# Optimization experiments

Hardware: AMD Instinct MI355X
Metric: run time of the kernel (lower is better)

The kernel has to match this reference:

```python
import jax, jax.numpy as jnp
import numpy as np

B, T, D, S = 64, 577, 768, 577  # batch, seq, hidden, v-out (=seq of e)


def setup_inputs() -> dict:
    key = jax.random.key(0)
    ks = jax.random.split(key, 8)
    sc = 1.0 / np.sqrt(D)
    return {
        "b": jax.random.normal(ks[0], (B, T, D), jnp.float32),
        "e": jax.random.normal(ks[1], (B, T, D), jnp.float32),
        "Wq": jax.random.normal(ks[2], (D, D), jnp.float32) * sc,
        "bq": jnp.zeros((D,), jnp.float32),
        "Wk": jax.random.normal(ks[3], (D, D), jnp.float32) * sc,
        "bk": jnp.zeros((D,), jnp.float32),
        "Wv": jax.random.normal(ks[4], (S, D), jnp.float32) * sc,
        "bv": jnp.zeros((S,), jnp.float32),
    }


def reference(b, e, Wq, bq, Wk, bk, Wv, bv):
    # Dropout layers are identity in eval mode.
    q = b @ Wq.T + bq                      # [B,T,D]
    k = e @ Wk.T + bk                      # [B,S,D]
    v = b @ Wv.T + bv                      # [B,T,S]
    # tanh(Q K^T) @ V^T : [B,T,S] @ [B,S,T] -> [B,T,T]
    attn = jnp.tanh(jnp.einsum("btd,bsd->bts", q, k))
    out = jnp.einsum("bts,bus->btu", attn, v)
    return out  # squeeze is a no-op for B>1
```

## Files before the change

### kernel.cpp

```cpp
#include <hip/hip_runtime.h>
#include <hip/hip_fp16.h>


typedef _Float16 f16x8 __attribute__((ext_vector_type(8)));
typedef _Float16 f16x4 __attribute__((ext_vector_type(4)));
typedef float f32x4 __attribute__((ext_vector_type(4)));

__global__ void cvt8_kernel(const float* __restrict__ src, _Float16* __restrict__ dst,
                            long long n8) {
    long long i = blockIdx.x * (long long)blockDim.x + threadIdx.x;
    const long long stride = gridDim.x * (long long)blockDim.x;
    for (; i < n8; i += stride) {
        const float4 f0 = ((const float4*)src)[2 * i];
        const float4 f1 = ((const float4*)src)[2 * i + 1];
        f16x8 h;
        h[0] = (_Float16)f0.x; h[1] = (_Float16)f0.y; h[2] = (_Float16)f0.z; h[3] = (_Float16)f0.w;
        h[4] = (_Float16)f1.x; h[5] = (_Float16)f1.y; h[6] = (_Float16)f1.z; h[7] = (_Float16)f1.w;
        ((f16x8*)dst)[i] = h;
    }
}

__global__ void cvtT2_kernel(const float* __restrict__ s0, _Float16* __restrict__ d0,
                             const float* __restrict__ s1, _Float16* __restrict__ d1) {
    __shared__ float t[32][33];
    const float* src = blockIdx.z ? s1 : s0;
    _Float16* dst = blockIdx.z ? d1 : d0;
    const int bx = blockIdx.x, by = blockIdx.y;
    const int tx = threadIdx.x & 31, ty = threadIdx.x >> 5;
#pragma unroll
    for (int k = 0; k < 4; ++k) {
        const int r = ty + 8 * k;
        t[r][tx] = src[(size_t)(by * 32 + r) * 768 + bx * 32 + tx];
    }
    __syncthreads();
#pragma unroll
    for (int k = 0; k < 4; ++k) {
        const int r = ty + 8 * k;
        dst[(size_t)(bx * 32 + r) * 768 + by * 32 + tx] = (_Float16)t[tx][r];
    }
}

__global__ void prep_kernel(const _Float16* __restrict__ WqT, const _Float16* __restrict__ WkT,
                            const float* __restrict__ bq, const float* __restrict__ bk,
                            const float* __restrict__ bv,
                            float* __restrict__ w2f, _Float16* __restrict__ Mt_aug,
                            float* __restrict__ bias_mg) {
    const int wid = blockIdx.x * 4 + (threadIdx.x >> 6);
    const int lane = threadIdx.x & 63;
    if (wid < 768) {
        float s = 0.f;
        for (int k = 0; k < 12; ++k) s += (float)WqT[(size_t)wid * 768 + lane + 64 * k] * bk[lane + 64 * k];
        for (int o = 32; o; o >>= 1) s += __shfl_xor(s, o);
        if (lane == 0) Mt_aug[(size_t)768 * 768 + wid] = (_Float16)s;
    } else if (wid < 1536) {
        const int n = wid - 768;
        float s = 0.f;
        for (int k = 0; k < 12; ++k) s += (float)WkT[(size_t)n * 768 + lane + 64 * k] * bq[lane + 64 * k];
        for (int o = 32; o; o >>= 1) s += __shfl_xor(s, o);
        if (lane == 0) w2f[n] = s;
    } else if (wid == 1536) {
        float s = 0.f;
        for (int k = 0; k < 12; ++k) s += bq[lane + 64 * k] * bk[lane + 64 * k];
        for (int o = 32; o; o >>= 1) s += __shfl_xor(s, o);
        if (lane < 32) {
            float v = 0.f;
            if (lane == 0) v = s;
            if (lane == 1) v = 1.f;
            bias_mg[768 + lane] = v;
        }
    } else if (wid < 1560) {
        const int i = (wid - 1537) * 64 + lane;
        if (i < 768) bias_mg[i] = 0.f;
        else {
            const int j = i + 32;
            if (j < 1408) bias_mg[j] = (j < 1377) ? bv[j - 800] : 0.f;
        }
    } else if (wid < 1591) {
        const int r = 769 + (wid - 1560);
        for (int k = 0; k < 12; ++k) Mt_aug[(size_t)r * 768 + lane + 64 * k] = (_Float16)0.f;
    }
}

__global__ void cvt_e_aug_kernel(const float* __restrict__ e, const float* __restrict__ w2f,
                                 _Float16* __restrict__ dst, int rows) {
    const int wpb = blockDim.x >> 6;
    int wid = blockIdx.x * wpb + (threadIdx.x >> 6);
    const int nw = gridDim.x * wpb;
    const int lane = threadIdx.x & 63;
    for (int s = wid; s < rows; s += nw) {
        const float4* er = (const float4*)(e + (size_t)s * 768);
        _Float16* dr = dst + (size_t)s * 800;
        float dot = 0.f;
#pragma unroll
        for (int k = 0; k < 3; ++k) {
            const int idx = lane + 64 * k;
            const float4 v = er[idx];
            const float4 w = ((const float4*)w2f)[idx];
            dot += v.x * w.x + v.y * w.y + v.z * w.z + v.w * w.w;
            f16x4 h;
            h[0] = (_Float16)v.x; h[1] = (_Float16)v.y;
            h[2] = (_Float16)v.z; h[3] = (_Float16)v.w;
            *(f16x4*)(dr + 4 * idx) = h;
        }
        for (int o = 32; o; o >>= 1) dot += __shfl_xor(dot, o);
        if (lane < 32) {
            _Float16 v = (_Float16)0.f;
            if (lane == 0) v = (_Float16)1.f;
            if (lane == 1) v = (_Float16)dot;
            dr[768 + lane] = v;
        }
    }
}

__device__ __forceinline__ void gload16(const _Float16* g, _Float16* l) {
    __builtin_amdgcn_global_load_lds(
        (const __attribute__((address_space(1))) unsigned int*)(g),
        (__attribute__((address_space(3))) unsigned int*)(l),
        16, 0, 0);
}

__device__ __forceinline__ float fast_tanh(float x) {
    const float t = __builtin_amdgcn_exp2f(2.885390081777927f * x);
    return 1.f - 2.f * __builtin_amdgcn_rcpf(t + 1.f);
}

template<bool TANH, bool OUT_F16, bool BIAS, int MODE>
__global__ __launch_bounds__(256)
void gemm_nt_f16(const _Float16* __restrict__ A, const _Float16* __restrict__ Bt,
                 const float* __restrict__ bias, void* __restrict__ Cp,
                 int M, int Nreal, int Nstore, int K,
                 int lda, int ldb, int ldc, int nTileN, int nTiles,
                 long long sA, long long sB, long long sC)
{
    __shared__ __align__(16) _Float16 lds[3 * 8192];

    int bid = blockIdx.x;
    int z, tm, tn;
    if (MODE == 0) {
        const int nwg = gridDim.x;
        const int q8 = nwg >> 3, r8 = nwg & 7;
        const int xcd = bid & 7, loc = bid >> 3;
        bid = (xcd < r8 ? xcd * (q8 + 1) : r8 * (q8 + 1) + (xcd - r8) * q8) + loc;
        z = 0;
        tm = bid / nTileN; tn = bid - tm * nTileN;
    } else {
        const int xcd = bid & 7, idx = bid >> 3;
        const int g = idx / nTiles, tile = idx - g * nTiles;
        z = g * 8 + xcd;
        tm = tile / nTileN; tn = tile - tm * nTileN;
    }
    const int m0 = tm << 7, n0 = tn << 7;

    const _Float16* Az = A + (size_t)z * sA;
    const _Float16* Bz = Bt + (size_t)z * sB;

    const int tid = threadIdx.x;
    const int lane = tid & 63;
    const int wid = tid >> 6;
    const int wm = wid >> 1, wn = wid & 1;

    const int r0 = tid >> 2;
    const int c0 = (((tid & 3) ^ ((tid >> 3) & 3)) << 3);
    const int rA0 = (m0 + r0      < M ? m0 + r0      : M - 1);
    const int rA1 = (m0 + r0 + 64 < M ? m0 + r0 + 64 : M - 1);
    const int rB0 = (n0 + r0      < Nreal ? n0 + r0      : Nreal - 1);
    const int rB1 = (n0 + r0 + 64 < Nreal ? n0 + r0 + 64 : Nreal - 1);
    const _Float16* pA0 = Az + (size_t)rA0 * lda + c0;
    const _Float16* pA1 = Az + (size_t)rA1 * lda + c0;
    const _Float16* pB0 = Bz + (size_t)rB0 * ldb + c0;
    const _Float16* pB1 = Bz + (size_t)rB1 * ldb + c0;

    const int o0 = tid * 8, o1 = (tid + 256) * 8;

    const int rr = lane & 15;
    const int hh = lane >> 4;
    const int sw = (rr >> 1) & 3;
    const int fAo = ((wm * 64 + rr) * 4 + (hh ^ sw)) * 8;
    const int fBo = ((wn * 64 + rr) * 4 + (hh ^ sw)) * 8;

    const f32x4 z4 = {0.f, 0.f, 0.f, 0.f};
    f32x4 acc[4][4];
#pragma unroll
    for (int i = 0; i < 4; ++i)
#pragma unroll
        for (int j = 0; j < 4; ++j) acc[i][j] = z4;

    const int nt = K >> 5;

#define STAGE(si, kt)                                              \
    do {                                                           \
        _Float16* base_ = lds + (si) * 8192;                       \
        const int ko_ = (kt) << 5;                                 \
        gload16(pA0 + ko_, base_ + o0);                            \
        gload16(pA1 + ko_, base_ + o1);                            \
        gload16(pB0 + ko_, base_ + 4096 + o0);                     \
        gload16(pB1 + ko_, base_ + 4096 + o1);                     \
    } while (0)

#define COMPUTE(si)                                                            \
    do {                                                                       \
        const _Float16* cA_ = lds + (si) * 8192;                               \
        const _Float16* cB_ = cA_ + 4096;                                      \
        f16x8 a_[4], b_[4];                                                    \
        _Pragma("unroll")                                                      \
        for (int mi = 0; mi < 4; ++mi) a_[mi] = *(const f16x8*)(cA_ + fAo + mi * 512); \
        _Pragma("unroll")                                                      \
        for (int ni = 0; ni < 4; ++ni) b_[ni] = *(const f16x8*)(cB_ + fBo + ni * 512); \
        _Pragma("unroll")                                                      \
        for (int mi = 0; mi < 4; ++mi)                                         \
            _Pragma("unroll")                                                  \
            for (int ni = 0; ni < 4; ++ni)                                     \
                acc[mi][ni] = __builtin_amdgcn_mfma_f32_16x16x32_f16(          \
                    a_[mi], b_[ni], acc[mi][ni], 0, 0, 0);                     \
    } while (0)

    STAGE(0, 0);
    STAGE(1, 1);

    for (int j = 0; j < nt - 1; ++j) {
        asm volatile("s_waitcnt vmcnt(4)" ::: "memory");
        __builtin_amdgcn_s_barrier();
        __builtin_amdgcn_sched_barrier(0);
        if (j + 2 < nt) STAGE((j + 2) % 3, j + 2);
        COMPUTE(j % 3);
    }
    asm volatile("s_waitcnt vmcnt(0)" ::: "memory");
    __builtin_amdgcn_s_barrier();
    __builtin_amdgcn_sched_barrier(0);
    COMPUTE((nt - 1) % 3);

#undef STAGE
#undef COMPUTE

    const int cr0 = (lane >> 4) << 2;
    const int cc = lane & 15;
    float*    Cf = (float*)Cp    + (size_t)z * sC;
    _Float16* Ch = (_Float16*)Cp + (size_t)z * sC;
#pragma unroll
    for (int mi = 0; mi < 4; ++mi) {
#pragma unroll
        for (int ni = 0; ni < 4; ++ni) {
            const int gc = n0 + wn * 64 + ni * 16 + cc;
            if (gc >= Nstore) continue;
            const bool real = gc < Nreal;
            float bb = 0.f;
            if (BIAS) bb = real ? bias[gc] : 0.f;
#pragma unroll
            for (int r = 0; r < 4; ++r) {
                const int gr = m0 + wm * 64 + mi * 16 + cr0 + r;
                if (gr >= M) continue;
                float x = real ? (acc[mi][ni][r] + bb) : 0.f;
                if (TANH) x = fast_tanh(x);
                if (OUT_F16) Ch[(size_t)gr * ldc + gc] = (_Float16)x;
                else         Cf[(size_t)gr * ldc + gc] = x;
            }
        }
    }
}

extern "C" void kernel_launch(void* const* d_in, const int* in_sizes, int n_in,
                              void* d_out, int out_size, void* d_ws, size_t ws_size,
                              hipStream_t stream)
{
    const float* b  = (const float*)d_in[0];
    const float* e  = (const float*)d_in[1];
    const float* Wq = (const float*)d_in[2];
    const float* bq = (const float*)d_in[3];
    const float* Wk = (const float*)d_in[4];
    const float* bk = (const float*)d_in[5];
    const float* Wv = (const float*)d_in[6];
    const float* bv = (const float*)d_in[7];
    float* out = (float*)d_out;

    const int BT = 36928, T = 577, S = 577, Sp = 608, Kb = 800;
    const int Nmg = 1408;

    _Float16* WqT_h  = (_Float16*)d_ws;
    _Float16* WkT_h  = WqT_h + 589824;
    _Float16* Mt_aug = WkT_h + 589824;
    _Float16* Wv_h   = Mt_aug + 614400;
    float*    bias_mg = (float*)(Wv_h + 443136);
    float*    w2f     = (float*)((_Float16*)bias_mg + 2816);
    _Float16* S1    = (_Float16*)w2f + 1536;
    _Float16* S_big = S1 + (size_t)BT * Kb;
    _Float16* S4    = S_big + (size_t)BT * Nmg;

    cvtT2_kernel<<<dim3(24, 24, 2), 256, 0, stream>>>(Wq, WqT_h, Wk, WkT_h);
    cvt8_kernel<<<217, 256, 0, stream>>>(Wv, Wv_h, 55392);
    prep_kernel<<<398, 256, 0, stream>>>(WqT_h, WkT_h, bq, bk, bv, w2f, Mt_aug, bias_mg);
    gemm_nt_f16<false, true, false, 0><<<dim3(36, 1, 1), 256, 0, stream>>>(
        WkT_h, WqT_h, nullptr, Mt_aug, 768, 768, 768, 768, 768, 768, 768, 6, 0, 0, 0, 0);

    cvt8_kernel<<<2048, 256, 0, stream>>>(b, S1, 3545088);
    gemm_nt_f16<false, true, true, 0><<<dim3(3179, 1, 1), 256, 0, stream>>>(
        S1, Mt_aug, bias_mg, S_big, BT, 1377, Nmg, 768, 768, 768, Nmg, 11, 0, 0, 0, 0);
    cvt_e_aug_kernel<<<2048, 256, 0, stream>>>(e, w2f, S1, BT);
    gemm_nt_f16<true, true, false, 1><<<dim3(1600, 1, 1), 256, 0, stream>>>(
        S_big, S1, nullptr, S4, T, S, Sp, Kb, Nmg, Kb, Sp, 5, 25,
        (long long)T * Nmg, (long long)T * Kb, (long long)T * Sp);
    gemm_nt_f16<false, false, false, 1><<<dim3(1600, 1, 1), 256, 0, stream>>>(
        S4, S_big + 800, nullptr, out, T, T, T, Sp, Sp, Nmg, T, 5, 25,
        (long long)T * Sp, (long long)T * Nmg, (long long)T * T);
}
```

Measured before the change: 346.0 us.

## Use 256x128-tile 512-thread GEMM for the large projection stage

```diff
diff --git a/kernel.cpp b/kernel.cpp
--- a/kernel.cpp
+++ b/kernel.cpp
@@ -124,6 +124,121 @@
     return 1.f - 2.f * __builtin_amdgcn_rcpf(t + 1.f);
 }
 
+__global__ __launch_bounds__(512)
+void gemm256m(const _Float16* __restrict__ A, const _Float16* __restrict__ Bt,
+              const float* __restrict__ bias, _Float16* __restrict__ C,
+              int M, int Nreal, int Nstore, int K,
+              int lda, int ldb, int ldc, int nTileN)
+{
+    __shared__ __align__(16) _Float16 lds[3 * 12288];
+
+    int bid = blockIdx.x;
+    {
+        const int nwg = gridDim.x;
+        const int q8 = nwg >> 3, r8 = nwg & 7;
+        const int xcd = bid & 7, loc = bid >> 3;
+        bid = (xcd < r8 ? xcd * (q8 + 1) : r8 * (q8 + 1) + (xcd - r8) * q8) + loc;
+    }
+    const int tm = bid / nTileN, tn = bid - tm * nTileN;
+    const int m0 = tm << 8, n0 = tn << 7;
+
+    const int tid = threadIdx.x;
+    const int lane = tid & 63;
+    const int wid = tid >> 6;
+    const int wm = wid >> 1;
+    const int wn = wid & 1;
+
+    const int r0 = tid >> 2;
+    const int c0 = (((tid & 3) ^ ((tid >> 3) & 3)) << 3);
+    int ra0 = m0 + r0;        if (ra0 >= M) ra0 = M - 1;
+    int ra1 = m0 + 128 + r0;  if (ra1 >= M) ra1 = M - 1;
+    int rb0 = n0 + r0;        if (rb0 >= Nreal) rb0 = Nreal - 1;
+    const _Float16* pA0 = A + (size_t)ra0 * lda + c0;
+    const _Float16* pA1 = A + (size_t)ra1 * lda + c0;
+    const _Float16* pB0 = Bt + (size_t)rb0 * ldb + c0;
+
+    const int o0 = tid * 8, o1 = (tid + 512) * 8;
+
+    const int rr = lane & 15;
+    const int hh = lane >> 4;
+    const int sw = (rr >> 1) & 3;
+    const int fAo = ((wm * 64 + rr) * 4 + (hh ^ sw)) * 8;
+    const int fBo = ((wn * 64 + rr) * 4 + (hh ^ sw)) * 8;
+
+    const f32x4 z4 = {0.f, 0.f, 0.f, 0.f};
+    f32x4 acc[4][4];
+#pragma unroll
+    for (int i = 0; i < 4; ++i)
+#pragma unroll
+        for (int j = 0; j < 4; ++j) acc[i][j] = z4;
+
+    const int nt = K >> 5;
+
+#define STAGE(si, kt)                                              \
+    do {                                                           \
+        _Float16* base_ = lds + (si) * 12288;                      \
+        const int ko_ = (kt) << 5;                                 \
+        gload16(pA0 + ko_, base_ + o0);                            \
+        gload16(pA1 + ko_, base_ + o1);                            \
+        gload16(pB0 + ko_, base_ + 8192 + o0);                     \
+    } while (0)
+
+#define COMPUTE(si)                                                            \
+    do {                                                                       \
+        const _Float16* cA_ = lds + (si) * 12288;                              \
+        const _Float16* cB_ = cA_ + 8192;                                      \
+        f16x8 a_[4], b_[4];                                                    \
+        _Pragma("unroll")                                                      \
+        for (int mi = 0; mi < 4; ++mi) a_[mi] = *(const f16x8*)(cA_ + fAo + mi * 512); \
+        _Pragma("unroll")                                                      \
+        for (int ni = 0; ni < 4; ++ni) b_[ni] = *(const f16x8*)(cB_ + fBo + ni * 512); \
+        _Pragma("unroll")                                                      \
+        for (int mi = 0; mi < 4; ++mi)                                         \
+            _Pragma("unroll")                                                  \
+            for (int ni = 0; ni < 4; ++ni)                                     \
+                acc[mi][ni] = __builtin_amdgcn_mfma_f32_16x16x32_f16(          \
+                    a_[mi], b_[ni], acc[mi][ni], 0, 0, 0);                     \
+    } while (0)
+
+    STAGE(0, 0);
+    STAGE(1, 1);
+
+    for (int j = 0; j < nt - 1; ++j) {
+        asm volatile("s_waitcnt vmcnt(3)" ::: "memory");
+        __builtin_amdgcn_s_barrier();
+        __builtin_amdgcn_sched_barrier(0);
+        if (j + 2 < nt) STAGE((j + 2) % 3, j + 2);
+        COMPUTE(j % 3);
+    }
+    asm volatile("s_waitcnt vmcnt(0)" ::: "memory");
+    __builtin_amdgcn_s_barrier();
+    __builtin_amdgcn_sched_barrier(0);
+    COMPUTE((nt - 1) % 3);
+
+#undef STAGE
+#undef COMPUTE
+
+    const int cr0 = (lane >> 4) << 2;
+    const int cc = lane & 15;
+#pragma unroll
+    for (int mi = 0; mi < 4; ++mi) {
+#pragma unroll
+        for (int ni = 0; ni < 4; ++ni) {
+            const int gc = n0 + wn * 64 + ni * 16 + cc;
+            if (gc >= Nstore) continue;
+            const bool real = gc < Nreal;
+            const float bb = real ? bias[gc] : 0.f;
+#pragma unroll
+            for (int r = 0; r < 4; ++r) {
+                const int gr = m0 + wm * 64 + mi * 16 + cr0 + r;
+                if (gr >= M) continue;
+                const float x = real ? (acc[mi][ni][r] + bb) : 0.f;
+                C[(size_t)gr * ldc + gc] = (_Float16)x;
+            }
+        }
+    }
+}
+
 template<bool TANH, bool OUT_F16, bool BIAS, int MODE>
 __global__ __launch_bounds__(256)
 void gemm_nt_f16(const _Float16* __restrict__ A, const _Float16* __restrict__ Bt,
@@ -292,8 +407,8 @@
         WkT_h, WqT_h, nullptr, Mt_aug, 768, 768, 768, 768, 768, 768, 768, 6, 0, 0, 0, 0);
 
     cvt8_kernel<<<2048, 256, 0, stream>>>(b, S1, 3545088);
-    gemm_nt_f16<false, true, true, 0><<<dim3(3179, 1, 1), 256, 0, stream>>>(
-        S1, Mt_aug, bias_mg, S_big, BT, 1377, Nmg, 768, 768, 768, Nmg, 11, 0, 0, 0, 0);
+    gemm256m<<<dim3(1595, 1, 1), 512, 0, stream>>>(
+        S1, Mt_aug, bias_mg, S_big, BT, 1377, Nmg, 768, 768, 768, Nmg, 11);
     cvt_e_aug_kernel<<<2048, 256, 0, stream>>>(e, w2f, S1, BT);
     gemm_nt_f16<true, true, false, 1><<<dim3(1600, 1, 1), 256, 0, stream>>>(
         S_big, S1, nullptr, S4, T, S, Sp, Kb, Nmg, Kb, Sp, 5, 25,
```

Measured after the change: 338.3 us, median of 2. -2.2%, faster.
